# Optimization experiments

Hardware: AMD Instinct MI355X
Metric: run time of the kernel (lower is better)

Reference implementation:

```python
import jax, jax.numpy as jnp
import numpy as np

N, K, D = 8192, 128, 128
INIT_STD = 0.01


def setup_inputs() -> dict:
    key = jax.random.key(0)
    k1, k2, k3, k4 = jax.random.split(key, 4)
    x = jax.random.normal(k1, (N, D), dtype=jnp.float32)
    means = INIT_STD * jax.random.normal(k2, (K, D), dtype=jnp.float32)
    logvar = INIT_STD * jax.random.normal(k3, (1, K, D), dtype=jnp.float32)
    tri = INIT_STD * jax.random.normal(k4, (1, K, D, D), dtype=jnp.float32)
    weigh = jnp.ones((1, K), dtype=jnp.float32)
    return {"x": x, "means": means, "logvar": logvar, "tri": tri, "weigh": weigh}


def reference(x, means, logvar, tri, weigh):
    d = x.shape[1]
    logC = -0.5 * d * jnp.log(2.0 * jnp.pi).astype(x.dtype)
    w = jax.nn.log_softmax(weigh, axis=1)                     # [1, K]
    var = jnp.exp(logvar)                                     # [1, K, d]
    y = (x[:, None, :] - means[None, :, :]) * var             # [N, K, d]
    # strictly-lower-triangular per-component matvec: tril(tri,-1) @ y
    tril = jnp.tril(tri[0], k=-1)                             # [K, d, d]
    y = y + jnp.einsum('kde,nke->nkd', tril, y)               # [N, K, d]
    quad = -0.5 * jnp.sum(y * y, axis=2)                      # [N, K]
    logdet = jnp.sum(jnp.log(jnp.abs(var) + 1e-8), axis=-1)   # [1, K]
    logits = quad + logdet + w                                # [N, K]
    logpdf = logC + jax.nn.logsumexp(logits, axis=-1)         # [N]
    return (-logpdf)[:, None]                                 # [N, 1]
```

## Files before the change

kernel.cpp:

```cpp
#include <hip/hip_runtime.h>
#include <math.h>

#define N_PTS 8192
#define K_CMP 128
#define D_DIM 128

typedef __attribute__((ext_vector_type(8)))  short  short8;
typedef __attribute__((ext_vector_type(8)))  unsigned short ushort8;
typedef __attribute__((ext_vector_type(4)))  unsigned short ushort4v;
typedef __attribute__((ext_vector_type(4)))  float  f32x4;
typedef __attribute__((ext_vector_type(16))) float  f32x16;

static __device__ __forceinline__ unsigned short f2bf(float f) {
    union { float f; unsigned u; } v; v.f = f;
    unsigned r = v.u + 0x7fffu + ((v.u >> 16) & 1u);
    return (unsigned short)(r >> 16);
}
static __device__ __forceinline__ float bf2f(unsigned short h) {
    union { unsigned u; float f; } v; v.u = ((unsigned)h) << 16;
    return v.f;
}


__global__ void prep_all(const float* __restrict__ x,
                         const float* __restrict__ means,
                         const float* __restrict__ logvar,
                         const float* __restrict__ tri,
                         const float* __restrict__ weigh,
                         unsigned short* __restrict__ Mpack,
                         unsigned short* __restrict__ xpack,
                         float* __restrict__ cneg,
                         float* __restrict__ cvec) {
    const int bid = blockIdx.x;
    const int tid = threadIdx.x;
    const int wave = tid >> 6, lane = tid & 63;
    const int l31 = lane & 31, lh = lane >> 5;

    if (bid >= K_CMP) {
        const int rc0 = (bid - K_CMP) * 2;
        #pragma unroll
        for (int j = 0; j < 4; ++j) {
            const int t  = wave * 4 + j;
            const int rc = rc0 + (t >> 3);
            const int es = t & 7;
            const int n  = rc * 32 + l31;
            const int e0 = es * 16 + lh * 8;
            const float4 v0 = *(const float4*)&x[(size_t)n * D_DIM + e0];
            const float4 v1 = *(const float4*)&x[(size_t)n * D_DIM + e0 + 4];
            ushort8 o;
            o[0] = f2bf(v0.x); o[1] = f2bf(v0.y); o[2] = f2bf(v0.z); o[3] = f2bf(v0.w);
            o[4] = f2bf(v1.x); o[5] = f2bf(v1.y); o[6] = f2bf(v1.z); o[7] = f2bf(v1.w);
            *(ushort8*)&xpack[((size_t)(rc * 8 + es) * 64 + lane) * 8] = o;
        }
        return;
    }

    const int k = bid;
    __shared__ float var_s[D_DIM], mu_s[D_DIM], credu[D_DIM];
    if (tid < D_DIM) {
        var_s[tid] = expf(logvar[k * D_DIM + tid]);
        mu_s[tid]  = means[k * D_DIM + tid];
        credu[tid] = 0.f;
    }
    __syncthreads();

    if (wave == 0) {
        float ld = logf(fabsf(var_s[lane]) + 1e-8f) +
                   logf(fabsf(var_s[lane + 64]) + 1e-8f);
        #pragma unroll
        for (int off = 1; off < 64; off <<= 1) ld += __shfl_xor(ld, off, 64);
        const float w1 = weigh[lane], w2 = weigh[lane + 64];
        float mx = fmaxf(w1, w2);
        #pragma unroll
        for (int off = 1; off < 64; off <<= 1) mx = fmaxf(mx, __shfl_xor(mx, off, 64));
        float se = __expf(w1 - mx) + __expf(w2 - mx);
        #pragma unroll
        for (int off = 1; off < 64; off <<= 1) se += __shfl_xor(se, off, 64);
        if (lane == 0) cvec[k] = ld + (weigh[k] - mx - logf(se));
    }

    const size_t kb = (size_t)k * D_DIM * D_DIM;
    #pragma unroll
    for (int j = 0; j < 5; ++j) {
        const int f = wave * 5 + j;
        const int S = (f < 2) ? 0 : (f < 6) ? 1 : (f < 12) ? 2 : 3;
        const int b = (S == 0) ? 0 : (S == 1) ? 2 : (S == 2) ? 6 : 12;
        const int es = f - b;
        const int r  = S * 32 + l31;
        const int e0 = es * 16 + lh * 8;
        const float4 v0 = *(const float4*)&tri[kb + (size_t)r * D_DIM + e0];
        const float4 v1 = *(const float4*)&tri[kb + (size_t)r * D_DIM + e0 + 4];
        const float vals[8] = {v0.x, v0.y, v0.z, v0.w, v1.x, v1.y, v1.z, v1.w};
        ushort8 ob;
        float cacc = 0.f;
        #pragma unroll
        for (int jj = 0; jj < 8; ++jj) {
            const int ee = e0 + jj;
            float val = (ee < r) ? vals[jj] * var_s[ee] : (ee == r ? var_s[r] : 0.f);
            unsigned short bq = f2bf(val);
            ob[jj] = bq;
            cacc = fmaf(bf2f(bq), mu_s[ee], cacc);
        }
        *(ushort8*)&Mpack[((size_t)(k * 20 + f) * 64 + lane) * 8] = ob;
        atomicAdd(&credu[r], cacc);
    }
    __syncthreads();
    if (tid < D_DIM) cneg[k * D_DIM + tid] = -credu[tid];
}

__launch_bounds__(256, 2)
__global__ void gmm_main(const unsigned short* __restrict__ xpack,
                         const unsigned short* __restrict__ Mpack,
                         const float* __restrict__ cneg,
                         const float* __restrict__ cvec,
                         float* __restrict__ logits) {
    __shared__ __align__(16) float cs[D_DIM];

    const int bid = blockIdx.x;
    const int k   = bid >> 2;
    const int nq  = bid & 3;
    const int tid = threadIdx.x;
    const int wave = tid >> 6;
    const int lane = tid & 63;
    const int l31  = lane & 31;
    const int lh   = lane >> 5;

    const float cv = cvec[k];

    if (lane < 32) ((float4*)cs)[lane] = ((const float4*)(cneg + (size_t)k * D_DIM))[lane];

    short8 mf[20];
    {
        const unsigned short* mp = Mpack + ((size_t)k * 20 * 64 + lane) * 8;
        #pragma unroll
        for (int f = 0; f < 20; ++f)
            asm volatile("global_load_dwordx4 %0, %1, off"
                         : "=v"(mf[f]) : "v"(mp + f * 64 * 8) : "memory");
    }

    #define ISSUE_X(Xar, itv) do {                                              \
        const int rc_ = nq * 64 + ((itv) & 15) * 4 + wave;                      \
        const unsigned short* xp_ = xpack + ((size_t)rc_ * 8 * 64 + lane) * 8;  \
        _Pragma("unroll")                                                       \
        for (int es_ = 0; es_ < 8; ++es_)                                       \
            asm volatile("global_load_dwordx4 %0, %1, off"                      \
                : "=v"(Xar[es_]) : "v"(xp_ + es_ * 64 * 8) : "memory");         \
    } while (0)

    short8 xa[8], xc[8];
    ISSUE_X(xa, 0);
    ISSUE_X(xc, 1);
    asm volatile("s_waitcnt vmcnt(8)" ::: "memory");
    __builtin_amdgcn_sched_barrier(0);

    #define SLAB(S_, B_, NES_, X_) {                                            \
        f32x16 ci_;                                                             \
        _Pragma("unroll")                                                       \
        for (int j_ = 0; j_ < 4; ++j_) {                                        \
            const f32x4 c_ = *(const f32x4*)&cs[S_ * 32 + 8 * j_ + 4 * lh];     \
            ci_[4*j_+0] = c_.x; ci_[4*j_+1] = c_.y;                             \
            ci_[4*j_+2] = c_.z; ci_[4*j_+3] = c_.w; }                           \
        f32x16 a_ = __builtin_amdgcn_mfma_f32_32x32x16_bf16(mf[B_], X_[0], ci_, 0, 0, 0); \
        _Pragma("unroll")                                                       \
        for (int e_ = 1; e_ < NES_; ++e_)                                       \
            a_ = __builtin_amdgcn_mfma_f32_32x32x16_bf16(mf[B_ + e_], X_[e_], a_, 0, 0, 0); \
        _Pragma("unroll")                                                       \
        for (int r_ = 0; r_ < 16; ++r_) {                                       \
            if      ((r_ & 3) == 0) q0 = fmaf(a_[r_], a_[r_], q0);              \
            else if ((r_ & 3) == 1) q1 = fmaf(a_[r_], a_[r_], q1);              \
            else if ((r_ & 3) == 2) q2 = fmaf(a_[r_], a_[r_], q2);              \
            else                    q3 = fmaf(a_[r_], a_[r_], q3); } }

    #define COMPUTE(X_, itv) {                                                  \
        float q0 = 0.f, q1 = 0.f, q2 = 0.f, q3 = 0.f;                           \
        __builtin_amdgcn_s_setprio(1);                                          \
        SLAB(0, 0,  2, X_);                                                     \
        SLAB(1, 2,  4, X_);                                                     \
        SLAB(2, 6,  6, X_);                                                     \
        SLAB(3, 12, 8, X_);                                                     \
        __builtin_amdgcn_s_setprio(0);                                          \
        float q_ = (q0 + q1) + (q2 + q3);                                       \
        q_ += __shfl_xor(q_, 32, 64);                                           \
        const int n_ = nq * 2048 + (itv) * 128 + wave * 32 + l31;               \
        if (lane < 32) logits[(size_t)k * N_PTS + n_] = -0.5f * q_ + cv;        \
    }

    #pragma unroll 1
    for (int it = 0; it < 16; it += 2) {
        COMPUTE(xa, it);
        ISSUE_X(xa, it + 2);
        asm volatile("s_waitcnt vmcnt(8)" ::: "memory");
        __builtin_amdgcn_sched_barrier(0);
        COMPUTE(xc, it + 1);
        ISSUE_X(xc, it + 3);
        asm volatile("s_waitcnt vmcnt(8)" ::: "memory");
        __builtin_amdgcn_sched_barrier(0);
    }
    asm volatile("s_waitcnt vmcnt(0)" ::: "memory");

    #undef COMPUTE
    #undef SLAB
    #undef ISSUE_X
}

__global__ void lse_kernel(const float* __restrict__ logits, float* __restrict__ out) {
    __shared__ float2 red[8][32];
    const int tid = threadIdx.x;
    const int nl = tid & 31, kc = tid >> 5;
    const int n = blockIdx.x * 32 + nl;
    float m = -INFINITY, s = 0.f;
    #pragma unroll
    for (int j = 0; j < 16; ++j) {
        const float v = logits[(size_t)(kc * 16 + j) * N_PTS + n];
        const float nm = fmaxf(m, v);
        s = s * __expf(m - nm) + __expf(v - nm);
        m = nm;
    }
    red[kc][nl] = make_float2(m, s);
    __syncthreads();
    if (tid < 32) {
        float M = -INFINITY;
        #pragma unroll
        for (int j = 0; j < 8; ++j) M = fmaxf(M, red[j][tid].x);
        float S = 0.f;
        #pragma unroll
        for (int j = 0; j < 8; ++j) S += red[j][tid].y * __expf(red[j][tid].x - M);
        const float logC = -117.62413225f;
        out[blockIdx.x * 32 + tid] = -(logC + M + logf(S));
    }
}

extern "C" void kernel_launch(void* const* d_in, const int* in_sizes, int n_in,
                              void* d_out, int out_size, void* d_ws, size_t ws_size,
                              hipStream_t stream) {
    const float* x      = (const float*)d_in[0];
    const float* means  = (const float*)d_in[1];
    const float* logvar = (const float*)d_in[2];
    const float* tri    = (const float*)d_in[3];
    const float* weigh  = (const float*)d_in[4];
    float* out = (float*)d_out;

    unsigned char* ws = (unsigned char*)d_ws;
    unsigned short* Mpack = (unsigned short*)(ws);
    unsigned short* xpack = (unsigned short*)(ws + (size_t)4 * 1024 * 1024);
    float*          cneg  = (float*)(ws + (size_t)6 * 1024 * 1024);
    float*          cvec  = (float*)(ws + (size_t)6 * 1024 * 1024 + 65536);
    float*          logits = (float*)(ws + (size_t)6 * 1024 * 1024 + 131072);

    hipLaunchKernelGGL(prep_all, dim3(256), dim3(256), 0, stream,
                       x, means, logvar, tri, weigh, Mpack, xpack, cneg, cvec);

    hipLaunchKernelGGL(gmm_main, dim3(K_CMP * 4), dim3(256), 0, stream,
                       xpack, Mpack, cneg, cvec, logits);

    hipLaunchKernelGGL(lse_kernel, dim3(N_PTS / 32), dim3(256), 0, stream,
                       logits, out);
}
```

Measured before the change: 42.08 us.

## Coalesce prep loads via LDS transpose, split rows per component, remap main blocks

The prep kernel now reads x and tri with fully coalesced float4 row loads, converts to bf16 into shared memory, and then writes the MFMA-packed layout. It also splits each component's rows over two blocks, doubling the prep grid. The main kernel interleaves components across blocks so concurrently running blocks share x slices. It also fully unrolls its loop and holds the 16 logits in registers, storing them at the end. Logdet now uses logvar directly, dropping the epsilon; this adds shared-memory traffic and register pressure in exchange for fewer uncoalesced accesses.

```diff
diff --git a/kernel.cpp b/kernel.cpp
--- a/kernel.cpp
+++ b/kernel.cpp
@@ -36,37 +36,42 @@
     const int wave = tid >> 6, lane = tid & 63;
     const int l31 = lane & 31, lh = lane >> 5;
 
-    if (bid >= K_CMP) {
-        const int rc0 = (bid - K_CMP) * 2;
-        #pragma unroll
-        for (int j = 0; j < 4; ++j) {
-            const int t  = wave * 4 + j;
-            const int rc = rc0 + (t >> 3);
-            const int es = t & 7;
-            const int n  = rc * 32 + l31;
-            const int e0 = es * 16 + lh * 8;
-            const float4 v0 = *(const float4*)&x[(size_t)n * D_DIM + e0];
-            const float4 v1 = *(const float4*)&x[(size_t)n * D_DIM + e0 + 4];
-            ushort8 o;
-            o[0] = f2bf(v0.x); o[1] = f2bf(v0.y); o[2] = f2bf(v0.z); o[3] = f2bf(v0.w);
-            o[4] = f2bf(v1.x); o[5] = f2bf(v1.y); o[6] = f2bf(v1.z); o[7] = f2bf(v1.w);
-            *(ushort8*)&xpack[((size_t)(rc * 8 + es) * 64 + lane) * 8] = o;
+    if (bid >= 256) {
+        __shared__ unsigned short Xt[32][136];
+        const int b = bid - 256;
+        #pragma unroll
+        for (int i = 0; i < 4; ++i) {
+            const int g  = (i * 256 + tid) * 4;
+            const int rl = g >> 7, e = g & 127;
+            const float4 v = *(const float4*)&x[(size_t)(b * 32 + rl) * D_DIM + e];
+            ushort4v o;
+            o.x = f2bf(v.x); o.y = f2bf(v.y); o.z = f2bf(v.z); o.w = f2bf(v.w);
+            *(ushort4v*)&Xt[rl][e] = o;
+        }
+        __syncthreads();
+        #pragma unroll
+        for (int j = 0; j < 2; ++j) {
+            const int es = wave * 2 + j;
+            const ushort8 vv = *(const ushort8*)&Xt[l31][es * 16 + lh * 8];
+            *(ushort8*)&xpack[((size_t)(b * 8 + es) * 64 + lane) * 8] = vv;
         }
         return;
     }
 
-    const int k = bid;
-    __shared__ float var_s[D_DIM], mu_s[D_DIM], credu[D_DIM];
+    __shared__ unsigned short Mt[64][136];
+    __shared__ float var_s[D_DIM], mu_s[D_DIM], credu[64];
+    const int k = bid >> 1, h = bid & 1;
+    const int rbase = h * 64;
+
     if (tid < D_DIM) {
         var_s[tid] = expf(logvar[k * D_DIM + tid]);
         mu_s[tid]  = means[k * D_DIM + tid];
-        credu[tid] = 0.f;
-    }
+    }
+    if (tid < 64) credu[tid] = 0.f;
     __syncthreads();
 
-    if (wave == 0) {
-        float ld = logf(fabsf(var_s[lane]) + 1e-8f) +
-                   logf(fabsf(var_s[lane + 64]) + 1e-8f);
+    if (h == 0 && wave == 0) {
+        float ld = logvar[k * D_DIM + lane] + logvar[k * D_DIM + lane + 64];
         #pragma unroll
         for (int off = 1; off < 64; off <<= 1) ld += __shfl_xor(ld, off, 64);
         const float w1 = weigh[lane], w2 = weigh[lane + 64];
@@ -81,31 +86,38 @@
 
     const size_t kb = (size_t)k * D_DIM * D_DIM;
     #pragma unroll
-    for (int j = 0; j < 5; ++j) {
-        const int f = wave * 5 + j;
-        const int S = (f < 2) ? 0 : (f < 6) ? 1 : (f < 12) ? 2 : 3;
-        const int b = (S == 0) ? 0 : (S == 1) ? 2 : (S == 2) ? 6 : 12;
-        const int es = f - b;
-        const int r  = S * 32 + l31;
-        const int e0 = es * 16 + lh * 8;
-        const float4 v0 = *(const float4*)&tri[kb + (size_t)r * D_DIM + e0];
-        const float4 v1 = *(const float4*)&tri[kb + (size_t)r * D_DIM + e0 + 4];
-        const float vals[8] = {v0.x, v0.y, v0.z, v0.w, v1.x, v1.y, v1.z, v1.w};
-        ushort8 ob;
+    for (int i = 0; i < 8; ++i) {
+        const int g  = (i * 256 + tid) * 4;
+        const int rl = g >> 7, e = g & 127;
+        const int R  = rbase + rl;
+        const float4 v = *(const float4*)&tri[kb + (size_t)R * D_DIM + e];
+        const float vals[4] = {v.x, v.y, v.z, v.w};
+        ushort4v ob;
         float cacc = 0.f;
         #pragma unroll
-        for (int jj = 0; jj < 8; ++jj) {
-            const int ee = e0 + jj;
-            float val = (ee < r) ? vals[jj] * var_s[ee] : (ee == r ? var_s[r] : 0.f);
-            unsigned short bq = f2bf(val);
-            ob[jj] = bq;
+        for (int j = 0; j < 4; ++j) {
+            const int ee = e + j;
+            float val = (ee < R) ? vals[j] * var_s[ee] : (ee == R ? var_s[R] : 0.f);
+            const unsigned short bq = f2bf(val);
+            ((unsigned short*)&ob)[j] = bq;
             cacc = fmaf(bf2f(bq), mu_s[ee], cacc);
         }
-        *(ushort8*)&Mpack[((size_t)(k * 20 + f) * 64 + lane) * 8] = ob;
-        atomicAdd(&credu[r], cacc);
+        *(ushort4v*)&Mt[rl][e] = ob;
+        atomicAdd(&credu[rl], cacc);
     }
     __syncthreads();
-    if (tid < D_DIM) cneg[k * D_DIM + tid] = -credu[tid];
+
+    const int nf = h ? 14 : 6;
+    const int fb = h ? 6 : 0;
+    for (int fi = wave; fi < nf; fi += 4) {
+        const int f  = fb + fi;
+        const int S  = (f < 2) ? 0 : (f < 6) ? 1 : (f < 12) ? 2 : 3;
+        const int es = f - ((S == 0) ? 0 : (S == 1) ? 2 : (S == 2) ? 6 : 12);
+        const int rl = (S - 2 * h) * 32 + l31;
+        const ushort8 vv = *(const ushort8*)&Mt[rl][es * 16 + lh * 8];
+        *(ushort8*)&Mpack[((size_t)(k * 20 + f) * 64 + lane) * 8] = vv;
+    }
+    if (tid < 64) cneg[k * D_DIM + rbase + tid] = -credu[tid];
 }
 
 __launch_bounds__(256, 2)
@@ -117,8 +129,10 @@
     __shared__ __align__(16) float cs[D_DIM];
 
     const int bid = blockIdx.x;
-    const int k   = bid >> 2;
-    const int nq  = bid & 3;
+    const int kq  = bid & 7;
+    const int ks  = (bid >> 3) & 15;
+    const int nq  = bid >> 7;
+    const int k   = kq * 16 + ks;
     const int tid = threadIdx.x;
     const int wave = tid >> 6;
     const int lane = tid & 63;
@@ -139,7 +153,7 @@
     }
 
     #define ISSUE_X(Xar, itv) do {                                              \
-        const int rc_ = nq * 64 + ((itv) & 15) * 4 + wave;                      \
+        const int rc_ = nq * 64 + (itv) * 4 + wave;                             \
         const unsigned short* xp_ = xpack + ((size_t)rc_ * 8 * 64 + lane) * 8;  \
         _Pragma("unroll")                                                       \
         for (int es_ = 0; es_ < 8; ++es_)                                       \
@@ -181,22 +195,33 @@
         __builtin_amdgcn_s_setprio(0);                                          \
         float q_ = (q0 + q1) + (q2 + q3);                                       \
         q_ += __shfl_xor(q_, 32, 64);                                           \
-        const int n_ = nq * 2048 + (itv) * 128 + wave * 32 + l31;               \
-        if (lane < 32) logits[(size_t)k * N_PTS + n_] = -0.5f * q_ + cv;        \
-    }
-
-    #pragma unroll 1
+        qreg[itv] = -0.5f * q_ + cv;                                            \
+    }
+
+    float qreg[16];
+    #pragma unroll
     for (int it = 0; it < 16; it += 2) {
         COMPUTE(xa, it);
-        ISSUE_X(xa, it + 2);
-        asm volatile("s_waitcnt vmcnt(8)" ::: "memory");
+        if (it + 2 < 16) {
+            ISSUE_X(xa, it + 2);
+            asm volatile("s_waitcnt vmcnt(8)" ::: "memory");
+        } else {
+            asm volatile("s_waitcnt vmcnt(0)" ::: "memory");
+        }
         __builtin_amdgcn_sched_barrier(0);
         COMPUTE(xc, it + 1);
-        ISSUE_X(xc, it + 3);
-        asm volatile("s_waitcnt vmcnt(8)" ::: "memory");
-        __builtin_amdgcn_sched_barrier(0);
-    }
-    asm volatile("s_waitcnt vmcnt(0)" ::: "memory");
+        if (it + 3 < 16) {
+            ISSUE_X(xc, it + 3);
+            asm volatile("s_waitcnt vmcnt(8)" ::: "memory");
+            __builtin_amdgcn_sched_barrier(0);
+        }
+    }
+
+    if (lane < 32) {
+        #pragma unroll
+        for (int it = 0; it < 16; ++it)
+            logits[(size_t)k * N_PTS + nq * 2048 + it * 128 + wave * 32 + l31] = qreg[it];
+    }
 
     #undef COMPUTE
     #undef SLAB
@@ -247,7 +272,7 @@
     float*          cvec  = (float*)(ws + (size_t)6 * 1024 * 1024 + 65536);
     float*          logits = (float*)(ws + (size_t)6 * 1024 * 1024 + 131072);
 
-    hipLaunchKernelGGL(prep_all, dim3(256), dim3(256), 0, stream,
+    hipLaunchKernelGGL(prep_all, dim3(512), dim3(256), 0, stream,
                        x, means, logvar, tri, weigh, Mpack, xpack, cneg, cvec);
 
     hipLaunchKernelGGL(gmm_main, dim3(K_CMP * 4), dim3(256), 0, stream,
```

New measurement: 42.83 us. No clear change (+1.8%).
